# Performance work log

Hardware: AMD Instinct MI355X
Metric: run time of the kernel (lower is better)

## Reference

```python
import jax, jax.numpy as jnp
import numpy as np

B, T, C, H = 8, 2048, 1024, 64  # batch, seq (block_size), n_embd, head_size


def setup_inputs() -> dict:
    key = jax.random.key(0)
    kx, kq, kk, kv = jax.random.split(key, 4)
    s = 1.0 / np.sqrt(C)
    return {
        "x": jax.random.normal(kx, (B, T, C), dtype=jnp.float32),
        "Wq": jax.random.normal(kq, (C, H), dtype=jnp.float32) * s,
        "Wk": jax.random.normal(kk, (C, H), dtype=jnp.float32) * s,
        "Wv": jax.random.normal(kv, (C, H), dtype=jnp.float32) * s,
    }


def reference(x, Wq, Wk, Wv):
    t = x.shape[1]
    q = jnp.einsum("btc,ch->bth", x, Wq)
    k = jnp.einsum("btc,ch->bth", x, Wk)
    v = jnp.einsum("btc,ch->bth", x, Wv)
    scores = jnp.einsum("bqh,bkh->bqk", q, k) / jnp.sqrt(jnp.float32(H))
    causal = jnp.tril(jnp.ones((t, t), dtype=bool))  # tril mask
    scores = jnp.where(causal, scores, -jnp.inf)
    attn = jax.nn.softmax(scores, axis=-1)
    return jnp.einsum("bqk,bkh->bqh", attn, v)
```

## Files before the change

kernel.cpp:

```cpp
#include <hip/hip_runtime.h>
#include <hip/hip_bf16.h>

#define BB 8
#define TT 2048
#define CC 1024
#define HH 64
#define NSPLIT 8

typedef __attribute__((ext_vector_type(8)))  short bf16x8;
typedef __attribute__((ext_vector_type(4)))  float f32x4;
typedef __attribute__((ext_vector_type(16))) float f32x16;
typedef __attribute__((ext_vector_type(8)))  unsigned short us8;
typedef __attribute__((ext_vector_type(4)))  unsigned short us4;
typedef unsigned int u32;

static __device__ __forceinline__ unsigned short f2bf(float f) {
    union { float f; unsigned int u; } v; v.f = f;
    unsigned int u = v.u;
    return (unsigned short)((u + 0x7FFFu + ((u >> 16) & 1u)) >> 16);
}
static __device__ __forceinline__ float bf2f(unsigned short s) {
    union { u32 u; float f; } v; v.u = ((u32)s) << 16; return v.f;
}

__global__ __launch_bounds__(256) void prep_weights(
        const float* __restrict__ Wq, const float* __restrict__ Wk,
        const float* __restrict__ Wv, unsigned short* __restrict__ Wt) {
    __shared__ float tile[64][65];
    int w  = blockIdx.x >> 4;
    int c0 = (blockIdx.x & 15) * 64;
    const float* W = (w == 0) ? Wq : (w == 1) ? Wk : Wv;
    int li = threadIdx.x;
    {
        int c = li >> 2, h4 = (li & 3) * 16;
        const float* src = W + (size_t)(c0 + c) * HH + h4;
        #pragma unroll
        for (int i = 0; i < 4; ++i) {
            float4 v4 = *(const float4*)(src + i * 4);
            tile[c][h4 + i*4 + 0] = v4.x; tile[c][h4 + i*4 + 1] = v4.y;
            tile[c][h4 + i*4 + 2] = v4.z; tile[c][h4 + i*4 + 3] = v4.w;
        }
    }
    __syncthreads();
    float scale = (w == 0) ? 0.1803368802f : 1.0f;
    int h = li >> 2, cg = (li & 3) * 16;
    unsigned short* dst = Wt + (size_t)w * HH * CC + (size_t)h * CC + c0 + cg;
    #pragma unroll
    for (int i = 0; i < 16; ++i) dst[i] = f2bf(tile[cg + i][h] * scale);
}

__global__ __launch_bounds__(512, 4) void proj_qkv(
        const float* __restrict__ x, const unsigned short* __restrict__ Wt,
        unsigned short* __restrict__ qws, unsigned short* __restrict__ kws,
        unsigned short* __restrict__ vws) {
    __shared__ unsigned short Xs[2][64 * 64];
    __shared__ unsigned short Ws[2][192 * 64];
    int tid = threadIdx.x;
    int wv = tid >> 6, lane = tid & 63;
    int quad = (lane >> 4) & 3, lq = lane & 15;
    int mg = wv >> 2, ng = wv & 3;
    int r0 = blockIdx.x * 64;

    int xr = tid >> 3, xg = tid & 7;
    const float* xsrc = x + (size_t)(r0 + xr) * CC + xg * 8;
    int xdst = xr * 64 + ((xg ^ (xr & 7)) * 8);
    float4 xa[2], xb[2];

    f32x4 acc[2][3];
    #pragma unroll
    for (int mt = 0; mt < 2; ++mt)
        #pragma unroll
        for (int nt = 0; nt < 3; ++nt)
            #pragma unroll
            for (int i = 0; i < 4; ++i) acc[mt][nt][i] = 0.0f;

    auto stageW = [&](int buf, int kc) {
        #pragma unroll
        for (int i = 0; i < 3; ++i) {
            int fp = tid + i * 512;
            int r = fp >> 3, pb = fp & 7, g = pb ^ (r & 7);
            const u32 __attribute__((address_space(1)))* gsrc =
                (const u32 __attribute__((address_space(1)))*)
                    (Wt + (size_t)r * CC + kc * 64 + g * 8);
            u32 __attribute__((address_space(3)))* ldst =
                (u32 __attribute__((address_space(3)))*)(&Ws[buf][fp * 8]);
            __builtin_amdgcn_global_load_lds(gsrc, ldst, 16, 0, 0);
        }
    };
    auto loadX = [&](int set, int kc) {
        xa[set] = *(const float4*)(xsrc + kc * 64);
        xb[set] = *(const float4*)(xsrc + kc * 64 + 4);
    };
    auto writeX = [&](int set, int buf) {
        unsigned short h[8];
        h[0]=f2bf(xa[set].x); h[1]=f2bf(xa[set].y);
        h[2]=f2bf(xa[set].z); h[3]=f2bf(xa[set].w);
        h[4]=f2bf(xb[set].x); h[5]=f2bf(xb[set].y);
        h[6]=f2bf(xb[set].z); h[7]=f2bf(xb[set].w);
        *(us8*)&Xs[buf][xdst] = *(const us8*)h;
    };

    loadX(0, 0); loadX(1, 1);
    stageW(0, 0);
    writeX(0, 0);

    for (int kc = 0; kc < 16; ++kc) {
        int cur = kc & 1;
        __syncthreads();
        if (kc < 15) stageW(1 - cur, kc + 1);
        if (kc < 14) loadX(kc & 1, kc + 2);
        #pragma unroll
        for (int ks = 0; ks < 2; ++ks) {
            int g = ks * 4 + quad;
            bf16x8 a[2], b[3];
            #pragma unroll
            for (int mt = 0; mt < 2; ++mt) {
                int arow = mg * 32 + mt * 16 + lq;
                a[mt] = *(const bf16x8*)&Xs[cur][arow * 64 + (g ^ (lq & 7)) * 8];
            }
            #pragma unroll
            for (int nt = 0; nt < 3; ++nt) {
                int brow = ng * 48 + nt * 16 + lq;
                b[nt] = *(const bf16x8*)&Ws[cur][brow * 64 + (g ^ (lq & 7)) * 8];
            }
            #pragma unroll
            for (int mt = 0; mt < 2; ++mt)
                #pragma unroll
                for (int nt = 0; nt < 3; ++nt)
                    acc[mt][nt] = __builtin_amdgcn_mfma_f32_16x16x32_bf16(
                        a[mt], b[nt], acc[mt][nt], 0, 0, 0);
        }
        if (kc < 15) writeX((kc + 1) & 1, 1 - cur);
    }

    int bidx = r0 >> 11;
    int t0base = r0 & (TT - 1);
    #pragma unroll
    for (int mt = 0; mt < 2; ++mt) {
        #pragma unroll
        for (int nt = 0; nt < 3; ++nt) {
            int gcol = ng * 48 + nt * 16 + lq;
            int rloc = mg * 32 + mt * 16 + quad * 4;
            if (gcol < 64) {
                #pragma unroll
                for (int i = 0; i < 4; ++i)
                    qws[(size_t)(r0 + rloc + i) * HH + gcol] =
                        f2bf(acc[mt][nt][i]);
            } else if (gcol < 128) {
                #pragma unroll
                for (int i = 0; i < 4; ++i)
                    kws[(size_t)(r0 + rloc + i) * HH + (gcol - 64)] =
                        f2bf(acc[mt][nt][i]);
            } else {
                unsigned short o[4];
                #pragma unroll
                for (int i = 0; i < 4; ++i) o[i] = f2bf(acc[mt][nt][i]);
                *(us4*)(vws + ((size_t)bidx * HH + (gcol - 128)) * TT
                            + t0base + rloc) = *(const us4*)o;
            }
        }
    }
}

__global__ __launch_bounds__(128, 3) void attn(
        const unsigned short* __restrict__ qws,
        const unsigned short* __restrict__ kws,
        const unsigned short* __restrict__ vws,
        unsigned short* __restrict__ Op, float* __restrict__ Lp) {
    __shared__ unsigned short Kt[32][72];
    __shared__ unsigned short Vt[64][40];
    __shared__ unsigned short Ps[64][40];
    int ti = blockIdx.x;
    int s  = blockIdx.y;
    int b  = blockIdx.z;
    int last = 2 * ti + 1;
    if (s > last) return;
    int tid = threadIdx.x, wv = tid >> 6, lane = tid & 63;
    int half = lane >> 5, l31 = lane & 31;

    bf16x8 qf[4];
    {
        const unsigned short* qp =
            qws + ((size_t)b * TT + ti * 64 + wv * 32 + l31) * HH + half * 8;
        #pragma unroll
        for (int ks = 0; ks < 4; ++ks) qf[ks] = *(const bf16x8*)(qp + ks * 16);
    }
    f32x16 O0, O1, Lc;
    #pragma unroll
    for (int i = 0; i < 16; ++i) { O0[i] = 0.f; O1[i] = 0.f; Lc[i] = 0.f; }
    bf16x8 ones;
    #pragma unroll
    for (int i = 0; i < 8; ++i) ones[i] = (short)0x3F80;

    int kr = tid >> 3, kg = tid & 7;
    int vh = tid >> 2, vkb = tid & 3;
    const unsigned short* ksrc0 = kws + ((size_t)b * TT + kr) * HH + kg * 8;
    const unsigned short* vsrc0 = vws + ((size_t)b * HH + vh) * TT + vkb * 8;

    us8 rk[2], rv[2];
    auto loadKV = [&](int jc) {
        rk[0] = *(const us8*)(ksrc0 + (size_t)(jc * 32) * HH);
        rk[1] = *(const us8*)(ksrc0 + (size_t)(jc * 32 + 16) * HH);
        rv[0] = *(const us8*)(vsrc0 + jc * 32);
        rv[1] = *(const us8*)(vsrc0 + (size_t)32 * TT + jc * 32);
    };
    auto writeKV = [&]() {
        *(us8*)&Kt[kr][kg * 8]       = rk[0];
        *(us8*)&Kt[kr + 16][kg * 8]  = rk[1];
        *(us8*)&Vt[vh][vkb * 8]      = rv[0];
        *(us8*)&Vt[vh + 32][vkb * 8] = rv[1];
    };

    loadKV(s);
    for (int jc = s; jc <= last; jc += NSPLIT) {
        __syncthreads();
        writeKV();
        if (jc + NSPLIT <= last) loadKV(jc + NSPLIT);
        __syncthreads();
        f32x16 S;
        #pragma unroll
        for (int i = 0; i < 16; ++i) S[i] = 0.f;
        #pragma unroll
        for (int ks = 0; ks < 4; ++ks) {
            bf16x8 kf = *(const bf16x8*)&Kt[l31][ks * 16 + half * 8];
            S = __builtin_amdgcn_mfma_f32_32x32x16_bf16(qf[ks], kf, S, 0, 0, 0);
        }
        bool diag = (jc >= 2 * ti + wv);
        #pragma unroll
        for (int r = 0; r < 16; ++r) {
            int pat = (r & 3) + 8 * (r >> 2) + 4 * half;
            float p = __builtin_amdgcn_exp2f(S[r]);
            if (diag && jc * 32 + l31 > ti * 64 + wv * 32 + pat) p = 0.0f;
            Ps[wv * 32 + pat][l31] = f2bf(p);
        }
        #pragma unroll
        for (int ks = 0; ks < 2; ++ks) {
            bf16x8 pa  = *(const bf16x8*)&Ps[wv * 32 + l31][ks * 16 + half * 8];
            bf16x8 vf0 = *(const bf16x8*)&Vt[l31][ks * 16 + half * 8];
            bf16x8 vf1 = *(const bf16x8*)&Vt[32 + l31][ks * 16 + half * 8];
            O0 = __builtin_amdgcn_mfma_f32_32x32x16_bf16(pa, vf0, O0, 0, 0, 0);
            O1 = __builtin_amdgcn_mfma_f32_32x32x16_bf16(pa, vf1, O1, 0, 0, 0);
            Lc = __builtin_amdgcn_mfma_f32_32x32x16_bf16(pa, ones, Lc, 0, 0, 0);
        }
    }
    unsigned short* Ob =
        Op + (((size_t)s * BB + b) * TT + ti * 64 + wv * 32) * HH;
    #pragma unroll
    for (int r = 0; r < 16; ++r) {
        int pat = (r & 3) + 8 * (r >> 2) + 4 * half;
        Ob[(size_t)pat * HH + l31]      = f2bf(O0[r]);
        Ob[(size_t)pat * HH + 32 + l31] = f2bf(O1[r]);
    }
    if (l31 == 0) {
        #pragma unroll
        for (int r = 0; r < 16; ++r) {
            int pat = (r & 3) + 8 * (r >> 2) + 4 * half;
            Lp[((size_t)s * BB + b) * TT + ti * 64 + wv * 32 + pat] = Lc[r];
        }
    }
}

__global__ __launch_bounds__(256) void norm_out(
        const unsigned short* __restrict__ Op, const float* __restrict__ Lp,
        float* __restrict__ out) {
    int idx = blockIdx.x * 256 + threadIdx.x;
    int g = idx >> 2;
    int hseg = (idx & 3) * 16;
    int ti = (g & (TT - 1)) >> 6;
    int ns = min(2 * ti + 2, NSPLIT);
    float a[16];
    #pragma unroll
    for (int j = 0; j < 16; ++j) a[j] = 0.f;
    float Ls = 0.f;
    for (int s = 0; s < ns; ++s) {
        const unsigned short* base =
            Op + ((size_t)s * BB * TT + g) * HH + hseg;
        us8 u0 = *(const us8*)base;
        us8 u1 = *(const us8*)(base + 8);
        #pragma unroll
        for (int j = 0; j < 8; ++j) { a[j] += bf2f(u0[j]); a[8 + j] += bf2f(u1[j]); }
        Ls += Lp[(size_t)s * BB * TT + g];
    }
    float inv = 1.0f / Ls;
    float* ob = out + (size_t)g * HH + hseg;
    #pragma unroll
    for (int q = 0; q < 4; ++q) {
        float4 v = make_float4(a[q*4] * inv, a[q*4+1] * inv,
                               a[q*4+2] * inv, a[q*4+3] * inv);
        ((float4*)ob)[q] = v;
    }
}

extern "C" void kernel_launch(void* const* d_in, const int* in_sizes, int n_in,
                              void* d_out, int out_size, void* d_ws, size_t ws_size,
                              hipStream_t stream) {
    (void)in_sizes; (void)n_in; (void)out_size; (void)ws_size;
    const float* x  = (const float*)d_in[0];
    const float* Wq = (const float*)d_in[1];
    const float* Wk = (const float*)d_in[2];
    const float* Wv = (const float*)d_in[3];
    float* out = (float*)d_out;

    char* ws = (char*)d_ws;
    unsigned short* Wt  = (unsigned short*)ws;
    unsigned short* qws = (unsigned short*)(ws + (1u << 19));
    unsigned short* kws = (unsigned short*)(ws + (1u << 19) + (1u << 21));
    unsigned short* vws = (unsigned short*)(ws + (1u << 19) + (2u << 21));
    unsigned short* Op  = (unsigned short*)(ws + (1u << 19) + (3u << 21));
    float*          Lp  = (float*)(ws + (1u << 19) + (3u << 21) + (1u << 24));

    prep_weights<<<48, 256, 0, stream>>>(Wq, Wk, Wv, Wt);
    proj_qkv<<<256, 512, 0, stream>>>(x, Wt, qws, kws, vws);
    attn<<<dim3(32, NSPLIT, 8), 128, 0, stream>>>(qws, kws, vws, Op, Lp);
    norm_out<<<256, 256, 0, stream>>>(Op, Lp, out);
}
```

Measured before the change: 136.3 us.

## Fuse split-K combine into attention via atomic last-block reduction; relax proj barrier waits

Drops the separate norm_out kernel. Each attention block now increments a per-tile atomic counter after writing its partial output, and the last split to finish sums the partials, divides by the row sums and writes the final output. In the projection loop, the full __syncthreads is replaced by an explicit s_waitcnt that leaves the next X global loads outstanding, followed by a raw barrier, so loads overlap compute. This saves one kernel launch and its drain, but adds threadfences, an atomic and a serialized tail reduction, and depends on prep_weights zeroing the counters.

```diff
diff --git a/kernel.cpp b/kernel.cpp
--- a/kernel.cpp
+++ b/kernel.cpp
@@ -25,12 +25,14 @@
 
 __global__ __launch_bounds__(256) void prep_weights(
         const float* __restrict__ Wq, const float* __restrict__ Wk,
-        const float* __restrict__ Wv, unsigned short* __restrict__ Wt) {
+        const float* __restrict__ Wv, unsigned short* __restrict__ Wt,
+        int* __restrict__ cnt) {
     __shared__ float tile[64][65];
     int w  = blockIdx.x >> 4;
     int c0 = (blockIdx.x & 15) * 64;
     const float* W = (w == 0) ? Wq : (w == 1) ? Wk : Wv;
     int li = threadIdx.x;
+    if (blockIdx.x == 0) cnt[li] = 0;
     {
         int c = li >> 2, h4 = (li & 3) * 16;
         const float* src = W + (size_t)(c0 + c) * HH + h4;
@@ -100,13 +102,16 @@
         *(us8*)&Xs[buf][xdst] = *(const us8*)h;
     };
 
+    stageW(0, 0);
     loadX(0, 0); loadX(1, 1);
-    stageW(0, 0);
     writeX(0, 0);
 
     for (int kc = 0; kc < 16; ++kc) {
         int cur = kc & 1;
-        __syncthreads();
+        if (kc < 15) asm volatile("s_waitcnt vmcnt(2) lgkmcnt(0)" ::: "memory");
+        else         asm volatile("s_waitcnt vmcnt(0) lgkmcnt(0)" ::: "memory");
+        __builtin_amdgcn_sched_barrier(0);
+        __builtin_amdgcn_s_barrier();
         if (kc < 15) stageW(1 - cur, kc + 1);
         if (kc < 14) loadX(kc & 1, kc + 2);
         #pragma unroll
@@ -166,10 +171,12 @@
         const unsigned short* __restrict__ qws,
         const unsigned short* __restrict__ kws,
         const unsigned short* __restrict__ vws,
-        unsigned short* __restrict__ Op, float* __restrict__ Lp) {
+        unsigned short* __restrict__ Op, float* __restrict__ Lp,
+        float* __restrict__ out, int* __restrict__ cnt) {
     __shared__ unsigned short Kt[32][72];
     __shared__ unsigned short Vt[64][40];
     __shared__ unsigned short Ps[64][40];
+    __shared__ int lastflag;
     int ti = blockIdx.x;
     int s  = blockIdx.y;
     int b  = blockIdx.z;
@@ -258,36 +265,43 @@
             Lp[((size_t)s * BB + b) * TT + ti * 64 + wv * 32 + pat] = Lc[r];
         }
     }
-}
-
-__global__ __launch_bounds__(256) void norm_out(
-        const unsigned short* __restrict__ Op, const float* __restrict__ Lp,
-        float* __restrict__ out) {
-    int idx = blockIdx.x * 256 + threadIdx.x;
-    int g = idx >> 2;
-    int hseg = (idx & 3) * 16;
-    int ti = (g & (TT - 1)) >> 6;
+
     int ns = min(2 * ti + 2, NSPLIT);
-    float a[16];
-    #pragma unroll
-    for (int j = 0; j < 16; ++j) a[j] = 0.f;
-    float Ls = 0.f;
-    for (int s = 0; s < ns; ++s) {
-        const unsigned short* base =
-            Op + ((size_t)s * BB * TT + g) * HH + hseg;
-        us8 u0 = *(const us8*)base;
-        us8 u1 = *(const us8*)(base + 8);
-        #pragma unroll
-        for (int j = 0; j < 8; ++j) { a[j] += bf2f(u0[j]); a[8 + j] += bf2f(u1[j]); }
-        Ls += Lp[(size_t)s * BB * TT + g];
-    }
-    float inv = 1.0f / Ls;
-    float* ob = out + (size_t)g * HH + hseg;
-    #pragma unroll
-    for (int q = 0; q < 4; ++q) {
-        float4 v = make_float4(a[q*4] * inv, a[q*4+1] * inv,
-                               a[q*4+2] * inv, a[q*4+3] * inv);
-        ((float4*)ob)[q] = v;
+    __threadfence();
+    __syncthreads();
+    if (tid == 0) {
+        int prev = atomicAdd(&cnt[b * 32 + ti], 1);
+        lastflag = (prev == ns - 1) ? 1 : 0;
+    }
+    __syncthreads();
+    if (lastflag) {
+        __threadfence();
+        int lr0 = tid >> 2, hb = (tid & 3) * 16;
+        #pragma unroll
+        for (int hf = 0; hf < 2; ++hf) {
+            size_t g = (size_t)b * TT + ti * 64 + hf * 32 + lr0;
+            float a[16];
+            #pragma unroll
+            for (int j = 0; j < 16; ++j) a[j] = 0.f;
+            float Ls = 0.f;
+            for (int s2 = 0; s2 < ns; ++s2) {
+                const unsigned short* base =
+                    Op + ((size_t)s2 * BB * TT + g) * HH + hb;
+                us8 u0 = *(const us8*)base;
+                us8 u1 = *(const us8*)(base + 8);
+                #pragma unroll
+                for (int j = 0; j < 8; ++j) {
+                    a[j] += bf2f(u0[j]); a[8 + j] += bf2f(u1[j]);
+                }
+                Ls += Lp[(size_t)s2 * BB * TT + g];
+            }
+            float inv = 1.0f / Ls;
+            float* ob = out + g * HH + hb;
+            #pragma unroll
+            for (int q = 0; q < 4; ++q)
+                ((float4*)ob)[q] = make_float4(a[q*4] * inv, a[q*4+1] * inv,
+                                               a[q*4+2] * inv, a[q*4+3] * inv);
+        }
     }
 }
 
@@ -308,9 +322,10 @@
     unsigned short* vws = (unsigned short*)(ws + (1u << 19) + (2u << 21));
     unsigned short* Op  = (unsigned short*)(ws + (1u << 19) + (3u << 21));
     float*          Lp  = (float*)(ws + (1u << 19) + (3u << 21) + (1u << 24));
-
-    prep_weights<<<48, 256, 0, stream>>>(Wq, Wk, Wv, Wt);
+    int*            cnt = (int*)(ws + (1u << 19) + (3u << 21) + (1u << 24)
+                                    + (1u << 19));
+
+    prep_weights<<<48, 256, 0, stream>>>(Wq, Wk, Wv, Wt, cnt);
     proj_qkv<<<256, 512, 0, stream>>>(x, Wt, qws, kws, vws);
-    attn<<<dim3(32, NSPLIT, 8), 128, 0, stream>>>(qws, kws, vws, Op, Lp);
-    norm_out<<<256, 256, 0, stream>>>(Op, Lp, out);
-}
+    attn<<<dim3(32, NSPLIT, 8), 128, 0, stream>>>(qws, kws, vws, Op, Lp, out, cnt);
+}
```

New measurement: 285.9 us. 110% more time.
